# Kernel optimization log

Measured on AMD Instinct MI355X. Metric: run time of the kernel, lower is better.

## Reference

```python
import jax, jax.numpy as jnp
import numpy as np

N_NODES = 19385
N_EDGES = 1_200_000
GNN = 256
HID = 512
RANK = 512
NCLS = 3
NGENES = 6640
NBLK = 6
B = 256
EPS = 1e-5


def _ln(x, g, b):
    m = jnp.mean(x, axis=-1, keepdims=True)
    v = jnp.mean(jnp.square(x - m), axis=-1, keepdims=True)
    return (x - m) * jax.lax.rsqrt(v + EPS) * g + b


def setup_inputs() -> dict:
    key = jax.random.key(0)
    ks = iter(jax.random.split(key, 40))
    w = lambda shape, s=0.02: jax.random.normal(next(ks), shape, jnp.float32) * s
    inp = {
        'node_idx': jax.random.randint(next(ks), (B,), -1, N_NODES),  # -1 == OOV
        'edge_index': jax.random.randint(next(ks), (2, N_EDGES), 0, N_NODES),
        'edge_weight': jax.random.uniform(next(ks), (N_EDGES,), jnp.float32),
        'frozen_emb': jax.random.normal(next(ks), (N_NODES, GNN), jnp.float32),
        # trainable partial GNN (mps.6, mps.7, post_mp)
        'conv6_W': w((GNN, GNN)), 'conv6_b': jnp.zeros((GNN,)),
        'ln6_g': jnp.ones((GNN,)), 'ln6_b': jnp.zeros((GNN,)),
        'conv7_W': w((GNN, GNN)), 'conv7_b': jnp.zeros((GNN,)),
        'ln7_g': jnp.ones((GNN,)), 'ln7_b': jnp.zeros((GNN,)),
        'post_W': w((GNN, GNN)), 'post_b': jnp.zeros((GNN,)),
        # head
        'oov_emb': w((GNN,)),
        'in_ln_g': jnp.ones((GNN,)), 'in_ln_b': jnp.zeros((GNN,)),
        'proj_in_W': w((GNN, HID)), 'proj_in_b': jnp.zeros((HID,)),
        'rb_ln_g': jnp.ones((NBLK, HID)), 'rb_ln_b': jnp.zeros((NBLK, HID)),
        'rb_W1': w((NBLK, HID, 4 * HID)), 'rb_b1': jnp.zeros((NBLK, 4 * HID)),
        'rb_W2': w((NBLK, 4 * HID, HID)), 'rb_b2': jnp.zeros((NBLK, HID)),
        'out_ln_g': jnp.ones((HID,)), 'out_ln_b': jnp.zeros((HID,)),
        'bil_W': w((HID, NCLS * RANK)), 'bil_b': jnp.zeros((NCLS * RANK,)),
        'out_gene_emb': w((NGENES, RANK)),
    }
    return inp


def reference(node_idx, edge_index, edge_weight, frozen_emb,
              conv6_W, conv6_b, ln6_g, ln6_b,
              conv7_W, conv7_b, ln7_g, ln7_b,
              post_W, post_b,
              oov_emb, in_ln_g, in_ln_b, proj_in_W, proj_in_b,
              rb_ln_g, rb_ln_b, rb_W1, rb_b1, rb_W2, rb_b2,
              out_ln_g, out_ln_b, bil_W, bil_b, out_gene_emb):
    src, dst = edge_index[0], edge_index[1]

    def conv(x, W, b):
        # edge-weighted message passing: gather -> scale -> scatter-add -> linear
        msg = x[src] * edge_weight[:, None]              # [E, GNN]
        agg = jax.ops.segment_sum(msg, dst, num_segments=N_NODES)
        return agg @ W + b

    # trainable GNN layers (eval mode: dropout = identity)
    x = frozen_emb
    x = x + jax.nn.relu(_ln(conv(x, conv6_W, conv6_b), ln6_g, ln6_b))
    x = x + jax.nn.relu(_ln(conv(x, conv7_W, conv7_b), ln7_g, ln7_b))
    node_emb = x @ post_W + post_b                       # [N, GNN]

    # OOV-aware lookup
    in_f = (node_idx >= 0).astype(jnp.float32)[:, None]  # [B,1]
    gnn_emb = node_emb[jnp.clip(node_idx, 0, None)]      # [B, GNN]
    h = gnn_emb * in_f + oov_emb[None, :] * (1.0 - in_f)

    # MLP head
    h = _ln(h, in_ln_g, in_ln_b) @ proj_in_W + proj_in_b
    for i in range(NBLK):
        t = _ln(h, rb_ln_g[i], rb_ln_b[i])
        t = jax.nn.gelu(t @ rb_W1[i] + rb_b1[i])
        h = h + t @ rb_W2[i] + rb_b2[i]
    h = _ln(h, out_ln_g, out_ln_b)

    pert = (h @ bil_W + bil_b).reshape(B, NCLS, RANK)
    logits = jnp.einsum('bcr,gr->bcg', pert, out_gene_emb)  # [B, 3, 6640]
    return logits
```

## Files before the change

### kernel.cpp

```cpp
#include <hip/hip_runtime.h>
#include <hip/hip_bf16.h>
#include <cstdint>
#include <cstddef>

#define N_NODES_C 19385
#define N_EDGES_C 1200000
#define GNN_C 256
#define HID_C 512
#define RANK_C 512
#define NCLS_C 3
#define NGENES_C 6640
#define NBLK_C 6
#define B_C 256
#define LN_EPS 1e-5f

#define PH_K 256
#define PH_CHUNK ((N_EDGES_C + PH_K - 1) / PH_K)
#define PH_NW ((N_NODES_C + 1) / 2)

typedef short bf8v __attribute__((ext_vector_type(8)));
typedef float f4v __attribute__((ext_vector_type(4)));
typedef int i2v __attribute__((ext_vector_type(2)));

__device__ __forceinline__ float bfu2f(unsigned short u) {
  union { unsigned int i; float f; } c; c.i = ((unsigned)u) << 16; return c.f;
}
__device__ __forceinline__ unsigned short f2bfu(float v) {
  union { float f; unsigned u; } c; c.f = v;
  unsigned r = c.u + 0x7FFFu + ((c.u >> 16) & 1u);
  return (unsigned short)(r >> 16);
}
__device__ __forceinline__ float gelu_tanh(float v) {
  const float x3 = v * v * v;
  return 0.5f * v * (1.f + tanhf(0.7978845608028654f * (v + 0.044715f * x3)));
}


struct CvtSeg { const float* s; unsigned short* d; long long n; };
struct CvtArgs { CvtSeg seg[2]; int nseg; };

__global__ __launch_bounds__(256) void multicvt_kernel(CvtArgs a) {
  for (int sg = 0; sg < a.nseg; ++sg) {
    const float4* s = reinterpret_cast<const float4*>(a.seg[sg].s);
    unsigned short* d = a.seg[sg].d;
    const long long n4 = a.seg[sg].n >> 2;
    for (long long i = blockIdx.x * 256 + threadIdx.x; i < n4;
         i += (long long)gridDim.x * 256) {
      float4 v = s[i];
      ushort4 o;
      o.x = f2bfu(v.x); o.y = f2bfu(v.y); o.z = f2bfu(v.z); o.w = f2bfu(v.w);
      *reinterpret_cast<ushort4*>(d + i * 4) = o;
    }
  }
}


struct TSeg { const float* s; unsigned short* d; int R, C; };
struct TArgs { TSeg seg[12]; int nseg; };

__global__ __launch_bounds__(256) void multitrans_kernel(TArgs a) {
  __shared__ float tile[32][33];
  const int tx = threadIdx.x & 31;
  const int ty = threadIdx.x >> 5;
  for (int sg = 0; sg < a.nseg; ++sg) {
    const int R = a.seg[sg].R, C = a.seg[sg].C;
    const int tC = C >> 5;
    const int nt = (R >> 5) * tC;
    const float* src = a.seg[sg].s;
    unsigned short* dst = a.seg[sg].d;
    for (int tid = blockIdx.x; tid < nt; tid += gridDim.x) {
      const int tr = tid / tC, tc = tid - tr * tC;
      const int r0 = tr * 32, c0 = tc * 32;
      __syncthreads();
#pragma unroll
      for (int j = 0; j < 32; j += 8)
        tile[ty + j][tx] = src[(size_t)(r0 + ty + j) * C + c0 + tx];
      __syncthreads();
#pragma unroll
      for (int j = 0; j < 32; j += 8)
        dst[(size_t)(c0 + ty + j) * R + r0 + tx] = f2bfu(tile[tx][ty + j]);
    }
  }
}


__global__ __launch_bounds__(256) void initmark_kernel(const int* __restrict__ node_idx,
                                                       int* __restrict__ selbm,
                                                       int* __restrict__ needed) {
  __shared__ int sel[B_C];
  sel[threadIdx.x] = max(node_idx[threadIdx.x], 0);
  __syncthreads();
  for (int i = blockIdx.x * 256 + threadIdx.x; i < N_NODES_C;
       i += gridDim.x * 256) {
    int m = 0;
#pragma unroll 16
    for (int j = 0; j < B_C; ++j) m |= (sel[j] == i);
    selbm[i] = m;
    needed[i] = m;
  }
}

__global__ __launch_bounds__(1024) void privhist_kernel(const int* __restrict__ src,
                                                        const int* __restrict__ dst,
                                                        const int* __restrict__ selbm,
                                                        int* __restrict__ needed,
                                                        unsigned int* __restrict__ cntp) {
  __shared__ unsigned int bins[PH_NW];
  const int t = threadIdx.x;
  for (int w = t; w < PH_NW; w += 1024) bins[w] = 0u;
  __syncthreads();
  const int base = blockIdx.x * PH_CHUNK;
  const int end = min(base + PH_CHUNK, N_EDGES_C);
#pragma unroll 2
  for (int i = base + t; i < end; i += 1024) {
    const int d = dst[i];
    atomicAdd(&bins[d >> 1], 1u << ((d & 1) * 16));
    if (selbm[d]) needed[src[i]] = 1;
  }
  __syncthreads();
  unsigned int* out = cntp + (size_t)blockIdx.x * PH_NW;
  for (int w = t; w < PH_NW; w += 1024) out[w] = bins[w];
}

__global__ __launch_bounds__(256) void redhist_kernel(unsigned int* __restrict__ cntp,
                                                      int* __restrict__ cnt) {
  const int w = blockIdx.x * 256 + threadIdx.x;
  if (w >= PH_NW) return;
  unsigned int lo = 0, hi = 0;
#pragma unroll 4
  for (int k = 0; k < PH_K; ++k) {
    const size_t idx = (size_t)k * PH_NW + w;
    const unsigned int u = cntp[idx];
    cntp[idx] = lo | (hi << 16);
    lo += u & 0xFFFFu;
    hi += u >> 16;
  }
  cnt[2 * w] = (int)lo;
  if (2 * w + 1 < N_NODES_C) cnt[2 * w + 1] = (int)hi;
}

__global__ __launch_bounds__(1024) void scan_kernel(const int* __restrict__ cnt,
                                                    int* __restrict__ off, int n) {
  __shared__ int sums[1024];
  const int t = threadIdx.x;
  const int CH = (n + 1023) >> 10;
  const int base = t * CH;
  int s = 0;
  for (int i = 0; i < CH; ++i) {
    int idx = base + i;
    if (idx < n) s += cnt[idx];
  }
  sums[t] = s;
  __syncthreads();
  for (int d = 1; d < 1024; d <<= 1) {
    int v = (t >= d) ? sums[t - d] : 0;
    __syncthreads();
    sums[t] += v;
    __syncthreads();
  }
  int run = (t == 0) ? 0 : sums[t - 1];
  for (int i = 0; i < CH; ++i) {
    int idx = base + i;
    if (idx < n) { off[idx] = run; run += cnt[idx]; }
  }
  if (t == 0) off[n] = sums[1023];
}

__global__ __launch_bounds__(1024) void fill_kernel(const int* __restrict__ src,
                                                    const int* __restrict__ dst,
                                                    const float* __restrict__ ew,
                                                    const int* __restrict__ off,
                                                    const unsigned int* __restrict__ cntp,
                                                    const int* __restrict__ needed,
                                                    i2v* __restrict__ ep) {
  __shared__ unsigned int bins[PH_NW];
  const int t = threadIdx.x;
  const unsigned int* myp = cntp + (size_t)blockIdx.x * PH_NW;
  for (int w = t; w < PH_NW; w += 1024) bins[w] = myp[w];
  __syncthreads();
  const int base = blockIdx.x * PH_CHUNK;
  const int end = min(base + PH_CHUNK, N_EDGES_C);
#pragma unroll 2
  for (int i = base + t; i < end; i += 1024) {
    const int d = dst[i];
    if (!needed[d]) continue;
    const int sh = (d & 1) * 16;
    const unsigned int old = atomicAdd(&bins[d >> 1], 1u << sh);
    const int rank = (int)((old >> sh) & 0xFFFFu);
    i2v e;
    e[0] = src[i] * GNN_C;
    e[1] = __float_as_int(ew[i]);
    ep[off[d] + rank] = e;
  }
}


__global__ __launch_bounds__(256) void agg_full_kernel(const i2v* __restrict__ ep,
                                                       const int* __restrict__ off,
                                                       const int* __restrict__ needed,
                                                       const unsigned short* __restrict__ x,
                                                       unsigned short* __restrict__ aggbf) {
  const int n = blockIdx.x;
  if (!needed[n]) return;
  __shared__ f4v red[4][64];
  const int t = threadIdx.x;
  const int w = __builtin_amdgcn_readfirstlane(t >> 6);
  const int lane = t & 63;
  const int s0 = off[n];
  const int c = off[n + 1] - s0;
  const int q0 = s0 + ((c * w) >> 2);
  const int q1 = s0 + ((c * (w + 1)) >> 2);
  float a0 = 0.f, a1 = 0.f, a2 = 0.f, a3 = 0.f;
  const unsigned short* xl = x + 4 * lane;
#pragma unroll 4
  for (int p = q0; p < q1; ++p) {
    const i2v e = ep[p];
    const int s = e[0];
    const float wg = __int_as_float(e[1]);
    const ushort4 v = *reinterpret_cast<const ushort4*>(xl + s);
    a0 = fmaf(bfu2f(v.x), wg, a0);
    a1 = fmaf(bfu2f(v.y), wg, a1);
    a2 = fmaf(bfu2f(v.z), wg, a2);
    a3 = fmaf(bfu2f(v.w), wg, a3);
  }
  f4v av; av[0] = a0; av[1] = a1; av[2] = a2; av[3] = a3;
  red[w][lane] = av;
  __syncthreads();
  const float* rf = reinterpret_cast<const float*>(red);
  const float sum = rf[t] + rf[256 + t] + rf[512 + t] + rf[768 + t];
  aggbf[(size_t)n * GNN_C + t] = f2bfu(sum);
}

__global__ __launch_bounds__(256) void agg_sel_kernel(const int* __restrict__ node_idx,
                                                      const i2v* __restrict__ ep,
                                                      const int* __restrict__ off,
                                                      const float* __restrict__ x,
                                                      unsigned short* __restrict__ aggbf) {
  __shared__ f4v red[4][64];
  const int b = blockIdx.x;
  const int t = threadIdx.x;
  const int n = max(node_idx[b], 0);
  const int w = __builtin_amdgcn_readfirstlane(t >> 6);
  const int lane = t & 63;
  const int s0 = off[n];
  const int c = off[n + 1] - s0;
  const int q0 = s0 + ((c * w) >> 2);
  const int q1 = s0 + ((c * (w + 1)) >> 2);
  float a0 = 0.f, a1 = 0.f, a2 = 0.f, a3 = 0.f;
  const float* xl = x + 4 * lane;
#pragma unroll 2
  for (int p = q0; p < q1; ++p) {
    const i2v e = ep[p];
    const int s = e[0];
    const float wg = __int_as_float(e[1]);
    const f4v v = *reinterpret_cast<const f4v*>(xl + s);
    a0 = fmaf(v[0], wg, a0);
    a1 = fmaf(v[1], wg, a1);
    a2 = fmaf(v[2], wg, a2);
    a3 = fmaf(v[3], wg, a3);
  }
  f4v av; av[0] = a0; av[1] = a1; av[2] = a2; av[3] = a3;
  red[w][lane] = av;
  __syncthreads();
  const float* rf = reinterpret_cast<const float*>(red);
  const float sum = rf[t] + rf[256 + t] + rf[512 + t] + rf[768 + t];
  aggbf[(size_t)b * GNN_C + t] = f2bfu(sum);
}


#define MBK 32
#define MLDW 40

__global__ __launch_bounds__(256) void mgemm_kernel(const unsigned short* __restrict__ A,
                                                    const unsigned short* __restrict__ Bt,
                                                    const float* __restrict__ bias,
                                                    float* __restrict__ C,
                                                    int M, int N, int K) {
  __shared__ unsigned short As[128][MLDW];
  __shared__ unsigned short Bs[128][MLDW];
  const int t = threadIdx.x;
  const int lane = t & 63;
  const int wave = t >> 6;
  const int r0 = blockIdx.x * 128;
  const int c0 = blockIdx.y * 128;
  const int wm = (wave >> 1) * 64;
  const int wn = (wave & 1) * 64;
  const int lm = lane & 15;
  const int lq = lane >> 4;

  f4v acc[4][4];
  for (int i = 0; i < 4; ++i)
    for (int j = 0; j < 4; ++j)
      for (int r = 0; r < 4; ++r) acc[i][j][r] = 0.f;

  const int row = t >> 1;
  const int kof = (t & 1) * 16;
  for (int k0 = 0; k0 < K; k0 += MBK) {
    {
      const int gr = r0 + row;
      uint4 u0 = make_uint4(0, 0, 0, 0), u1 = u0;
      if (gr < M) {
        const uint4* p = reinterpret_cast<const uint4*>(A + (size_t)gr * K + k0 + kof);
        u0 = p[0]; u1 = p[1];
      }
      *reinterpret_cast<uint4*>(&As[row][kof]) = u0;
      *reinterpret_cast<uint4*>(&As[row][kof + 8]) = u1;
    }
    {
      const int gn = c0 + row;
      uint4 u0 = make_uint4(0, 0, 0, 0), u1 = u0;
      if (gn < N) {
        const uint4* p = reinterpret_cast<const uint4*>(Bt + (size_t)gn * K + k0 + kof);
        u0 = p[0]; u1 = p[1];
      }
      *reinterpret_cast<uint4*>(&Bs[row][kof]) = u0;
      *reinterpret_cast<uint4*>(&Bs[row][kof + 8]) = u1;
    }
    __syncthreads();

    bf8v a[4], b[4];
#pragma unroll
    for (int i = 0; i < 4; ++i)
      a[i] = *reinterpret_cast<const bf8v*>(&As[wm + i * 16 + lm][lq * 8]);
#pragma unroll
    for (int j = 0; j < 4; ++j)
      b[j] = *reinterpret_cast<const bf8v*>(&Bs[wn + j * 16 + lm][lq * 8]);
#pragma unroll
    for (int i = 0; i < 4; ++i)
#pragma unroll
      for (int j = 0; j < 4; ++j)
        acc[i][j] = __builtin_amdgcn_mfma_f32_16x16x32_bf16(a[i], b[j], acc[i][j], 0, 0, 0);
    __syncthreads();
  }

  for (int ti = 0; ti < 4; ++ti) {
    for (int tj = 0; tj < 4; ++tj) {
      const int col = c0 + wn + tj * 16 + lm;
      if (col >= N) continue;
      const float bv = bias ? bias[col] : 0.f;
      for (int r = 0; r < 4; ++r) {
        const int row2 = r0 + wm + ti * 16 + lq * 4 + r;
        if (row2 < M) C[(size_t)row2 * N + col] = acc[ti][tj][r] + bv;
      }
    }
  }
}


__global__ __launch_bounds__(256) void mgemm32_kernel(const unsigned short* __restrict__ A,
                                                      const unsigned short* __restrict__ Bt,
                                                      const float* __restrict__ bias,
                                                      float* outF, unsigned short* outB,
                                                      int M, int N, int K, int doGelu) {
  __shared__ unsigned short As[32][MLDW];
  __shared__ unsigned short Bs[64][MLDW];
  const int t = threadIdx.x;
  const int lane = t & 63;
  const int wave = t >> 6;
  const int r0 = blockIdx.x * 32;
  const int c0 = blockIdx.y * 64;
  const int wn = wave * 16;
  const int lm = lane & 15;
  const int lq = lane >> 4;

  f4v acc[2];
#pragma unroll
  for (int i = 0; i < 2; ++i)
#pragma unroll
    for (int r = 0; r < 4; ++r) acc[i][r] = 0.f;

  const int arow = t >> 3, akof = (t & 7) * 4;
  const int brow = t >> 2, bkof = (t & 3) * 8;
  for (int k0 = 0; k0 < K; k0 += MBK) {
    *reinterpret_cast<ushort4*>(&As[arow][akof]) =
        *reinterpret_cast<const ushort4*>(A + (size_t)(r0 + arow) * K + k0 + akof);
    *reinterpret_cast<uint4*>(&Bs[brow][bkof]) =
        *reinterpret_cast<const uint4*>(Bt + (size_t)(c0 + brow) * K + k0 + bkof);
    __syncthreads();
    bf8v a[2], b;
#pragma unroll
    for (int i = 0; i < 2; ++i)
      a[i] = *reinterpret_cast<const bf8v*>(&As[i * 16 + lm][lq * 8]);
    b = *reinterpret_cast<const bf8v*>(&Bs[wn + lm][lq * 8]);
#pragma unroll
    for (int i = 0; i < 2; ++i)
      acc[i] = __builtin_amdgcn_mfma_f32_16x16x32_bf16(a[i], b, acc[i], 0, 0, 0);
    __syncthreads();
  }

  const int col = c0 + wn + lm;
  const float bv = bias ? bias[col] : 0.f;
#pragma unroll
  for (int ti = 0; ti < 2; ++ti)
#pragma unroll
    for (int r = 0; r < 4; ++r) {
      const int row2 = r0 + ti * 16 + lq * 4 + r;
      float v = acc[ti][r] + bv;
      if (doGelu) v = gelu_tanh(v);
      if (outF) outF[(size_t)row2 * N + col] = v;
      else outB[(size_t)row2 * N + col] = f2bfu(v);
    }
}

__global__ __launch_bounds__(256) void skmgemm32_kernel(const unsigned short* __restrict__ A,
                                                        const unsigned short* __restrict__ Bt,
                                                        float* __restrict__ part,
                                                        int M, int N, int K, int kc) {
  __shared__ unsigned short As[32][MLDW];
  __shared__ unsigned short Bs[64][MLDW];
  const int t = threadIdx.x;
  const int lane = t & 63;
  const int wave = t >> 6;
  const int r0 = blockIdx.x * 32;
  const int c0 = blockIdx.y * 64;
  const int kBeg = blockIdx.z * kc;
  const int kEnd = kBeg + kc;
  const int wn = wave * 16;
  const int lm = lane & 15;
  const int lq = lane >> 4;

  f4v acc[2];
#pragma unroll
  for (int i = 0; i < 2; ++i)
#pragma unroll
    for (int r = 0; r < 4; ++r) acc[i][r] = 0.f;

  const int arow = t >> 3, akof = (t & 7) * 4;
  const int brow = t >> 2, bkof = (t & 3) * 8;
  for (int k0 = kBeg; k0 < kEnd; k0 += MBK) {
    *reinterpret_cast<ushort4*>(&As[arow][akof]) =
        *reinterpret_cast<const ushort4*>(A + (size_t)(r0 + arow) * K + k0 + akof);
    *reinterpret_cast<uint4*>(&Bs[brow][bkof]) =
        *reinterpret_cast<const uint4*>(Bt + (size_t)(c0 + brow) * K + k0 + bkof);
    __syncthreads();
    bf8v a[2], b;
#pragma unroll
    for (int i = 0; i < 2; ++i)
      a[i] = *reinterpret_cast<const bf8v*>(&As[i * 16 + lm][lq * 8]);
    b = *reinterpret_cast<const bf8v*>(&Bs[wn + lm][lq * 8]);
#pragma unroll
    for (int i = 0; i < 2; ++i)
      acc[i] = __builtin_amdgcn_mfma_f32_16x16x32_bf16(a[i], b, acc[i], 0, 0, 0);
    __syncthreads();
  }

  float* out = part + (size_t)blockIdx.z * M * N;
  const int col = c0 + wn + lm;
#pragma unroll
  for (int ti = 0; ti < 2; ++ti)
#pragma unroll
    for (int r = 0; r < 4; ++r) {
      const int row2 = r0 + ti * 16 + lq * 4 + r;
      out[(size_t)row2 * N + col] = acc[ti][r];
    }
}

__global__ __launch_bounds__(512) void gemmln6_kernel(const unsigned short* __restrict__ A,
                                                      const unsigned short* __restrict__ Bt,
                                                      const float* __restrict__ bias,
                                                      const float* __restrict__ g,
                                                      const float* __restrict__ b,
                                                      const float* __restrict__ frozen,
                                                      const int* __restrict__ needed,
                                                      float* __restrict__ yx, int M) {
  __shared__ unsigned short As[32][MLDW];
  __shared__ unsigned short Bs[256][MLDW];
  __shared__ float rs[32][8];
  const int t = threadIdx.x;
  const int lane = t & 63;
  const int wave = t >> 6;
  const int r0 = blockIdx.x * 32;
  const int lm = lane & 15, lq = lane >> 4;

  f4v acc[2][2];
#pragma unroll
  for (int i = 0; i < 2; ++i)
#pragma unroll
    for (int j = 0; j < 2; ++j)
#pragma unroll
      for (int r = 0; r < 4; ++r) acc[i][j][r] = 0.f;

  const int arow = t >> 3, akof = (t & 7) * 4;
  for (int k0 = 0; k0 < GNN_C; k0 += MBK) {
    if (t < 256) {
      ushort4 u = make_ushort4(0, 0, 0, 0);
      const int gr = r0 + arow;
      if (gr < M) u = *reinterpret_cast<const ushort4*>(A + (size_t)gr * GNN_C + k0 + akof);
      *reinterpret_cast<ushort4*>(&As[arow][akof]) = u;
    }
#pragma unroll
    for (int j = 0; j < 2; ++j) {
      const int id = t + 512 * j;
      const int brow = id >> 2, bkof = (id & 3) * 8;
      *reinterpret_cast<uint4*>(&Bs[brow][bkof]) =
          *reinterpret_cast<const uint4*>(Bt + (size_t)brow * GNN_C + k0 + bkof);
    }
    __syncthreads();
    bf8v a[2], bf[2];
#pragma unroll
    for (int ti = 0; ti < 2; ++ti)
      a[ti] = *reinterpret_cast<const bf8v*>(&As[ti * 16 + lm][lq * 8]);
#pragma unroll
    for (int tj = 0; tj < 2; ++tj)
      bf[tj] = *reinterpret_cast<const bf8v*>(&Bs[wave * 32 + tj * 16 + lm][lq * 8]);
#pragma unroll
    for (int ti = 0; ti < 2; ++ti)
#pragma unroll
      for (int tj = 0; tj < 2; ++tj)
        acc[ti][tj] = __builtin_amdgcn_mfma_f32_16x16x32_bf16(a[ti], bf[tj], acc[ti][tj], 0, 0, 0);
    __syncthreads();
  }

  const int c0 = wave * 32 + lm, c1 = c0 + 16;
  const float b0 = bias[c0], b1 = bias[c1];
#pragma unroll
  for (int ti = 0; ti < 2; ++ti)
#pragma unroll
    for (int r = 0; r < 4; ++r) { acc[ti][0][r] += b0; acc[ti][1][r] += b1; }

  float m[2][4];
#pragma unroll
  for (int ti = 0; ti < 2; ++ti)
#pragma unroll
    for (int r = 0; r < 4; ++r) {
      float s = acc[ti][0][r] + acc[ti][1][r];
      for (int o = 1; o < 16; o <<= 1) s += __shfl_xor(s, o, 64);
      if (lm == 0) rs[ti * 16 + lq * 4 + r][wave] = s;
    }
  __syncthreads();
#pragma unroll
  for (int ti = 0; ti < 2; ++ti)
#pragma unroll
    for (int r = 0; r < 4; ++r) {
      const int row = ti * 16 + lq * 4 + r;
      float s = 0.f;
#pragma unroll
      for (int w2 = 0; w2 < 8; ++w2) s += rs[row][w2];
      m[ti][r] = s * (1.f / GNN_C);
    }
  __syncthreads();
  float iv[2][4];
#pragma unroll
  for (int ti = 0; ti < 2; ++ti)
#pragma unroll
    for (int r = 0; r < 4; ++r) {
      const float d0 = acc[ti][0][r] - m[ti][r];
      const float d1 = acc[ti][1][r] - m[ti][r];
      float s = d0 * d0 + d1 * d1;
      for (int o = 1; o < 16; o <<= 1) s += __shfl_xor(s, o, 64);
      if (lm == 0) rs[ti * 16 + lq * 4 + r][wave] = s;
    }
  __syncthreads();
#pragma unroll
  for (int ti = 0; ti < 2; ++ti)
#pragma unroll
    for (int r = 0; r < 4; ++r) {
      const int row = ti * 16 + lq * 4 + r;
      float s = 0.f;
#pragma unroll
      for (int w2 = 0; w2 < 8; ++w2) s += rs[row][w2];
      iv[ti][r] = rsqrtf(s * (1.f / GNN_C) + LN_EPS);
    }

  const float g0 = g[c0], g1 = g[c1], bb0 = b[c0], bb1 = b[c1];
#pragma unroll
  for (int ti = 0; ti < 2; ++ti)
#pragma unroll
    for (int r = 0; r < 4; ++r) {
      const int grow = r0 + ti * 16 + lq * 4 + r;
      if (grow < M && needed[grow]) {
        const size_t base = (size_t)grow * GNN_C;
        const float x0 = fmaxf((acc[ti][0][r] - m[ti][r]) * iv[ti][r] * g0 + bb0, 0.f);
        const float x1 = fmaxf((acc[ti][1][r] - m[ti][r]) * iv[ti][r] * g1 + bb1, 0.f);
        yx[base + c0] = frozen[base + c0] + x0;
        yx[base + c1] = frozen[base + c1] + x1;
      }
    }
}


__global__ __launch_bounds__(256) void postconv7_kernel(const float* __restrict__ y,
                                                        const float* __restrict__ g,
                                                        const float* __restrict__ b,
                                                        const int* __restrict__ idx,
                                                        const float* __restrict__ x1f,
                                                        unsigned short* __restrict__ out) {
  __shared__ float sb[4];
  const int bi = blockIdx.x, t = threadIdx.x;
  const int n = max(idx[bi], 0);
  const float v = y[(size_t)bi * GNN_C + t];
  float s = v;
  for (int o = 32; o; o >>= 1) s += __shfl_down(s, o, 64);
  if ((t & 63) == 0) sb[t >> 6] = s;
  __syncthreads();
  const float m = (sb[0] + sb[1] + sb[2] + sb[3]) * (1.f / GNN_C);
  __syncthreads();
  const float d = v - m;
  s = d * d;
  for (int o = 32; o; o >>= 1) s += __shfl_down(s, o, 64);
  if ((t & 63) == 0) sb[t >> 6] = s;
  __syncthreads();
  const float rs = rsqrtf((sb[0] + sb[1] + sb[2] + sb[3]) * (1.f / GNN_C) + LN_EPS);
  const float xn = d * rs * g[t] + b[t];
  out[(size_t)bi * GNN_C + t] = f2bfu(x1f[(size_t)n * GNN_C + t] + fmaxf(xn, 0.f));
}

__global__ __launch_bounds__(256) void h0ln_kernel(const float* __restrict__ ne,
                                                   const int* __restrict__ idx,
                                                   const float* __restrict__ oov,
                                                   const float* __restrict__ g,
                                                   const float* __restrict__ b,
                                                   unsigned short* __restrict__ out) {
  __shared__ float sb[4];
  const int bi = blockIdx.x, t = threadIdx.x;
  const float v = (idx[bi] >= 0) ? ne[(size_t)bi * GNN_C + t] : oov[t];
  float s = v;
  for (int o = 32; o; o >>= 1) s += __shfl_down(s, o, 64);
  if ((t & 63) == 0) sb[t >> 6] = s;
  __syncthreads();
  const float m = (sb[0] + sb[1] + sb[2] + sb[3]) * (1.f / GNN_C);
  __syncthreads();
  const float d = v - m;
  s = d * d;
  for (int o = 32; o; o >>= 1) s += __shfl_down(s, o, 64);
  if ((t & 63) == 0) sb[t >> 6] = s;
  __syncthreads();
  const float rs = rsqrtf((sb[0] + sb[1] + sb[2] + sb[3]) * (1.f / GNN_C) + LN_EPS);
  out[(size_t)bi * GNN_C + t] = f2bfu(d * rs * g[t] + b[t]);
}

__global__ __launch_bounds__(256) void lnbf_kernel(const float* __restrict__ in,
                                                   const float* __restrict__ g,
                                                   const float* __restrict__ b,
                                                   unsigned short* __restrict__ out) {
  __shared__ float sb[4];
  const int r = blockIdx.x, t = threadIdx.x;
  const float v0 = in[(size_t)r * HID_C + t];
  const float v1 = in[(size_t)r * HID_C + t + 256];
  float s = v0 + v1;
  for (int o = 32; o; o >>= 1) s += __shfl_down(s, o, 64);
  if ((t & 63) == 0) sb[t >> 6] = s;
  __syncthreads();
  const float m = (sb[0] + sb[1] + sb[2] + sb[3]) * (1.f / HID_C);
  __syncthreads();
  const float d0 = v0 - m, d1 = v1 - m;
  s = d0 * d0 + d1 * d1;
  for (int o = 32; o; o >>= 1) s += __shfl_down(s, o, 64);
  if ((t & 63) == 0) sb[t >> 6] = s;
  __syncthreads();
  const float rs = rsqrtf((sb[0] + sb[1] + sb[2] + sb[3]) * (1.f / HID_C) + LN_EPS);
  out[(size_t)r * HID_C + t] = f2bfu(d0 * rs * g[t] + b[t]);
  out[(size_t)r * HID_C + t + 256] = f2bfu(d1 * rs * g[t + 256] + b[t + 256]);
}

__global__ __launch_bounds__(256) void combln_kernel(const float* __restrict__ part,
                                                     float* __restrict__ h,
                                                     const float* __restrict__ b2,
                                                     const float* __restrict__ g,
                                                     const float* __restrict__ b,
                                                     unsigned short* __restrict__ out) {
  __shared__ float sb[4];
  const int r = blockIdx.x, t = threadIdx.x;
  const int MN = B_C * HID_C;
  const size_t o0 = (size_t)r * HID_C + t;
  const size_t o1 = o0 + 256;
  float v0 = h[o0] + b2[t] + part[o0] + part[MN + o0] + part[2 * MN + o0] + part[3 * MN + o0];
  float v1 = h[o1] + b2[t + 256] + part[o1] + part[MN + o1] + part[2 * MN + o1] + part[3 * MN + o1];
  h[o0] = v0;
  h[o1] = v1;
  float s = v0 + v1;
  for (int o = 32; o; o >>= 1) s += __shfl_down(s, o, 64);
  if ((t & 63) == 0) sb[t >> 6] = s;
  __syncthreads();
  const float m = (sb[0] + sb[1] + sb[2] + sb[3]) * (1.f / HID_C);
  __syncthreads();
  const float d0 = v0 - m, d1 = v1 - m;
  s = d0 * d0 + d1 * d1;
  for (int o = 32; o; o >>= 1) s += __shfl_down(s, o, 64);
  if ((t & 63) == 0) sb[t >> 6] = s;
  __syncthreads();
  const float rsq = rsqrtf((sb[0] + sb[1] + sb[2] + sb[3]) * (1.f / HID_C) + LN_EPS);
  out[o0] = f2bfu(d0 * rsq * g[t] + b[t]);
  out[o1] = f2bfu(d1 * rsq * g[t + 256] + b[t + 256]);
}


extern "C" void kernel_launch(void* const* d_in, const int* in_sizes, int n_in,
                              void* d_out, int out_size, void* d_ws, size_t ws_size,
                              hipStream_t stream) {
  const int* node_idx = (const int*)d_in[0];
  const int* e_src = (const int*)d_in[1];
  const int* e_dst = e_src + N_EDGES_C;
  const float* ew = (const float*)d_in[2];
  const float* frozen = (const float*)d_in[3];
  const float* W6 = (const float*)d_in[4];
  const float* b6 = (const float*)d_in[5];
  const float* g6 = (const float*)d_in[6];
  const float* bl6 = (const float*)d_in[7];
  const float* W7 = (const float*)d_in[8];
  const float* b7 = (const float*)d_in[9];
  const float* g7 = (const float*)d_in[10];
  const float* bl7 = (const float*)d_in[11];
  const float* postW = (const float*)d_in[12];
  const float* postb = (const float*)d_in[13];
  const float* oov = (const float*)d_in[14];
  const float* ing = (const float*)d_in[15];
  const float* inb = (const float*)d_in[16];
  const float* projW = (const float*)d_in[17];
  const float* projb = (const float*)d_in[18];
  const float* rbg = (const float*)d_in[19];
  const float* rbb = (const float*)d_in[20];
  const float* rbW1 = (const float*)d_in[21];
  const float* rbb1 = (const float*)d_in[22];
  const float* rbW2 = (const float*)d_in[23];
  const float* rbb2 = (const float*)d_in[24];
  const float* outg = (const float*)d_in[25];
  const float* outb = (const float*)d_in[26];
  const float* bilW = (const float*)d_in[27];
  const float* bilb = (const float*)d_in[28];
  const float* gene = (const float*)d_in[29];
  (void)in_sizes; (void)n_in; (void)out_size; (void)ws_size;

  char* ws = (char*)d_ws;
  size_t o = 0;
  auto alloc = [&](size_t bytes) -> char* {
    char* p = ws + o;
    o += (bytes + 255) & ~(size_t)255;
    return p;
  };
  int* cnt = (int*)alloc((size_t)N_NODES_C * 4);
  int* off = (int*)alloc((size_t)(N_NODES_C + 1) * 4);
  int* needed = (int*)alloc((size_t)N_NODES_C * 4);
  int* selbm = (int*)alloc((size_t)N_NODES_C * 4);
  unsigned int* cntp = (unsigned int*)alloc((size_t)PH_K * PH_NW * 4);
  i2v* ep = (i2v*)alloc((size_t)N_EDGES_C * 8);
  unsigned short* frozbf = (unsigned short*)alloc((size_t)N_NODES_C * GNN_C * 2);
  char* aggregion = alloc((size_t)NBLK_C * HID_C * 4 * HID_C * 2);
  unsigned short* w6t = (unsigned short*)alloc((size_t)GNN_C * GNN_C * 2);
  unsigned short* w7t = (unsigned short*)alloc((size_t)GNN_C * GNN_C * 2);
  unsigned short* postWt = (unsigned short*)alloc((size_t)GNN_C * GNN_C * 2);
  unsigned short* projWt = (unsigned short*)alloc((size_t)HID_C * GNN_C * 2);
  unsigned short* bilWt = (unsigned short*)alloc((size_t)NCLS_C * RANK_C * HID_C * 2);
  float* yx = (float*)alloc((size_t)N_NODES_C * GNN_C * 4);
  unsigned short* rbW2t = (unsigned short*)alloc((size_t)NBLK_C * 4 * HID_C * HID_C * 2);
  float* part = (float*)alloc((size_t)4 * B_C * HID_C * 4);
  unsigned short* agg7bf = (unsigned short*)alloc((size_t)B_C * GNN_C * 2);
  float* y7b = (float*)alloc((size_t)B_C * GNN_C * 4);
  unsigned short* x2bf = (unsigned short*)alloc((size_t)B_C * GNN_C * 2);
  float* nemb = (float*)alloc((size_t)B_C * GNN_C * 4);
  unsigned short* h0lbf = (unsigned short*)alloc((size_t)B_C * GNN_C * 2);
  float* h = (float*)alloc((size_t)B_C * HID_C * 4);
  unsigned short* tbf = (unsigned short*)alloc((size_t)B_C * HID_C * 2);
  unsigned short* ubf = (unsigned short*)alloc((size_t)B_C * 4 * HID_C * 2);
  unsigned short* pertbf = (unsigned short*)alloc((size_t)B_C * NCLS_C * RANK_C * 2);

  unsigned short* agg6bf = (unsigned short*)aggregion;
  unsigned short* rbW1t = (unsigned short*)aggregion;
  unsigned short* genebf = frozbf;

  initmark_kernel<<<80, 256, 0, stream>>>(node_idx, selbm, needed);
  privhist_kernel<<<PH_K, 1024, 0, stream>>>(e_src, e_dst, selbm, needed, cntp);
  redhist_kernel<<<(PH_NW + 255) / 256, 256, 0, stream>>>(cntp, cnt);
  scan_kernel<<<1, 1024, 0, stream>>>(cnt, off, N_NODES_C);
  fill_kernel<<<PH_K, 1024, 0, stream>>>(e_src, e_dst, ew, off, cntp, needed, ep);

  {
    CvtArgs a;
    a.seg[0] = {frozen, frozbf, (long long)N_NODES_C * GNN_C};
    a.nseg = 1;
    multicvt_kernel<<<512, 256, 0, stream>>>(a);
  }
  {
    TArgs a;
    a.seg[0] = {W6, w6t, GNN_C, GNN_C};
    a.seg[1] = {W7, w7t, GNN_C, GNN_C};
    a.seg[2] = {postW, postWt, GNN_C, GNN_C};
    a.seg[3] = {projW, projWt, GNN_C, HID_C};
    a.seg[4] = {bilW, bilWt, HID_C, NCLS_C * RANK_C};
    a.nseg = 5;
    multitrans_kernel<<<512, 256, 0, stream>>>(a);
  }

  agg_full_kernel<<<N_NODES_C, 256, 0, stream>>>(ep, off, needed, frozbf, agg6bf);
  gemmln6_kernel<<<(N_NODES_C + 31) / 32, 512, 0, stream>>>(agg6bf, w6t, b6, g6, bl6,
                                                            frozen, needed, yx, N_NODES_C);

  {
    TArgs a;
    for (int i = 0; i < NBLK_C; ++i) {
      a.seg[i] = {rbW1 + (size_t)i * HID_C * 4 * HID_C,
                  rbW1t + (size_t)i * HID_C * 4 * HID_C, HID_C, 4 * HID_C};
      a.seg[6 + i] = {rbW2 + (size_t)i * 4 * HID_C * HID_C,
                      rbW2t + (size_t)i * 4 * HID_C * HID_C, 4 * HID_C, HID_C};
    }
    a.nseg = 12;
    multitrans_kernel<<<2048, 256, 0, stream>>>(a);
  }
  {
    CvtArgs a;
    a.seg[0] = {gene, genebf, (long long)NGENES_C * RANK_C};
    a.nseg = 1;
    multicvt_kernel<<<512, 256, 0, stream>>>(a);
  }

  agg_sel_kernel<<<B_C, 256, 0, stream>>>(node_idx, ep, off, yx, agg7bf);
  {
    dim3 g(B_C / 32, GNN_C / 64);
    mgemm32_kernel<<<g, 256, 0, stream>>>(agg7bf, w7t, b7, y7b, nullptr,
                                          B_C, GNN_C, GNN_C, 0);
  }
  postconv7_kernel<<<B_C, 256, 0, stream>>>(y7b, g7, bl7, node_idx, yx, x2bf);

  {
    dim3 g(B_C / 32, GNN_C / 64);
    mgemm32_kernel<<<g, 256, 0, stream>>>(x2bf, postWt, postb, nemb, nullptr,
                                          B_C, GNN_C, GNN_C, 0);
  }
  h0ln_kernel<<<B_C, 256, 0, stream>>>(nemb, node_idx, oov, ing, inb, h0lbf);

  {
    dim3 g(B_C / 32, HID_C / 64);
    mgemm32_kernel<<<g, 256, 0, stream>>>(h0lbf, projWt, projb, h, nullptr,
                                          B_C, HID_C, GNN_C, 0);
  }
  lnbf_kernel<<<B_C, 256, 0, stream>>>(h, rbg, rbb, tbf);

  for (int i = 0; i < NBLK_C; ++i) {
    {
      dim3 g(B_C / 32, (4 * HID_C) / 64);
      mgemm32_kernel<<<g, 256, 0, stream>>>(tbf, rbW1t + (size_t)i * HID_C * 4 * HID_C,
                                            rbb1 + (size_t)i * 4 * HID_C, nullptr, ubf,
                                            B_C, 4 * HID_C, HID_C, 1);
    }
    {
      dim3 g(B_C / 32, HID_C / 64, 4);
      skmgemm32_kernel<<<g, 256, 0, stream>>>(ubf, rbW2t + (size_t)i * 4 * HID_C * HID_C,
                                              part, B_C, HID_C, 4 * HID_C, HID_C);
    }
    const float* gn = (i < NBLK_C - 1) ? rbg + (size_t)(i + 1) * HID_C : outg;
    const float* bn = (i < NBLK_C - 1) ? rbb + (size_t)(i + 1) * HID_C : outb;
    combln_kernel<<<B_C, 256, 0, stream>>>(part, h, rbb2 + (size_t)i * HID_C, gn, bn, tbf);
  }

  {
    dim3 g(B_C / 32, (NCLS_C * RANK_C) / 64);
    mgemm32_kernel<<<g, 256, 0, stream>>>(tbf, bilWt, bilb, nullptr, pertbf,
                                          B_C, NCLS_C * RANK_C, HID_C, 0);
  }

  {
    dim3 g((B_C * NCLS_C) / 128, (NGENES_C + 127) / 128);
    mgemm_kernel<<<g, 256, 0, stream>>>(pertbf, genebf, nullptr, (float*)d_out,
                                        B_C * NCLS_C, NGENES_C, RANK_C);
  }
}
```

Baseline: 551.6 us.

## Fuse residual MLP stack into one cooperative kernel with grid syncs

Replaces the 18 per-block kernel launches (W1 GEMM+GELU, split-K W2 GEMM, combine+LayerNorm) with a single cooperative kernel of 256 blocks that loops over the six residual blocks and separates the stages with grid-wide barriers. The aim is to remove launch overhead and inter-kernel gaps for these small GEMMs. In exchange it adds grid.sync cost, and the launch depends on all 256 blocks being co-resident. The launch return value is ignored.

```diff
diff --git a/kernel.cpp b/kernel.cpp
--- a/kernel.cpp
+++ b/kernel.cpp
@@ -1,7 +1,10 @@
 #include <hip/hip_runtime.h>
 #include <hip/hip_bf16.h>
+#include <hip/hip_cooperative_groups.h>
 #include <cstdint>
 #include <cstddef>
+
+namespace cg = cooperative_groups;
 
 #define N_NODES_C 19385
 #define N_EDGES_C 1200000
@@ -402,57 +405,125 @@
     }
 }
 
-__global__ __launch_bounds__(256) void skmgemm32_kernel(const unsigned short* __restrict__ A,
-                                                        const unsigned short* __restrict__ Bt,
-                                                        float* __restrict__ part,
-                                                        int M, int N, int K, int kc) {
+__global__ __launch_bounds__(256) void resstack_kernel(
+    unsigned short* __restrict__ tbf, unsigned short* __restrict__ ubf,
+    float* __restrict__ part, float* __restrict__ h,
+    const unsigned short* __restrict__ rbW1t, const float* __restrict__ rbb1,
+    const unsigned short* __restrict__ rbW2t, const float* __restrict__ rbb2,
+    const float* __restrict__ rbg, const float* __restrict__ rbb,
+    const float* __restrict__ outg, const float* __restrict__ outb) {
   __shared__ unsigned short As[32][MLDW];
   __shared__ unsigned short Bs[64][MLDW];
+  __shared__ float sb[4];
+  cg::grid_group grid = cg::this_grid();
   const int t = threadIdx.x;
   const int lane = t & 63;
   const int wave = t >> 6;
-  const int r0 = blockIdx.x * 32;
-  const int c0 = blockIdx.y * 64;
-  const int kBeg = blockIdx.z * kc;
-  const int kEnd = kBeg + kc;
+  const int lm = lane & 15, lq = lane >> 4;
   const int wn = wave * 16;
-  const int lm = lane & 15;
-  const int lq = lane >> 4;
-
-  f4v acc[2];
-#pragma unroll
-  for (int i = 0; i < 2; ++i)
-#pragma unroll
-    for (int r = 0; r < 4; ++r) acc[i][r] = 0.f;
-
+  const int blk = blockIdx.x;
   const int arow = t >> 3, akof = (t & 7) * 4;
   const int brow = t >> 2, bkof = (t & 3) * 8;
-  for (int k0 = kBeg; k0 < kEnd; k0 += MBK) {
-    *reinterpret_cast<ushort4*>(&As[arow][akof]) =
-        *reinterpret_cast<const ushort4*>(A + (size_t)(r0 + arow) * K + k0 + akof);
-    *reinterpret_cast<uint4*>(&Bs[brow][bkof]) =
-        *reinterpret_cast<const uint4*>(Bt + (size_t)(c0 + brow) * K + k0 + bkof);
-    __syncthreads();
-    bf8v a[2], b;
-#pragma unroll
-    for (int i = 0; i < 2; ++i)
-      a[i] = *reinterpret_cast<const bf8v*>(&As[i * 16 + lm][lq * 8]);
-    b = *reinterpret_cast<const bf8v*>(&Bs[wn + lm][lq * 8]);
-#pragma unroll
-    for (int i = 0; i < 2; ++i)
-      acc[i] = __builtin_amdgcn_mfma_f32_16x16x32_bf16(a[i], b, acc[i], 0, 0, 0);
-    __syncthreads();
-  }
-
-  float* out = part + (size_t)blockIdx.z * M * N;
-  const int col = c0 + wn + lm;
-#pragma unroll
-  for (int ti = 0; ti < 2; ++ti)
-#pragma unroll
-    for (int r = 0; r < 4; ++r) {
-      const int row2 = r0 + ti * 16 + lq * 4 + r;
-      out[(size_t)row2 * N + col] = acc[ti][r];
-    }
+
+  for (int i = 0; i < NBLK_C; ++i) {
+    {
+      const unsigned short* W1 = rbW1t + (size_t)i * HID_C * 4 * HID_C;
+      const float* b1 = rbb1 + (size_t)i * 4 * HID_C;
+      const int r0 = (blk >> 5) * 32;
+      const int c0 = (blk & 31) * 64;
+      f4v acc[2];
+#pragma unroll
+      for (int q = 0; q < 2; ++q)
+#pragma unroll
+        for (int r = 0; r < 4; ++r) acc[q][r] = 0.f;
+      for (int k0 = 0; k0 < HID_C; k0 += MBK) {
+        *reinterpret_cast<ushort4*>(&As[arow][akof]) =
+            *reinterpret_cast<const ushort4*>(tbf + (size_t)(r0 + arow) * HID_C + k0 + akof);
+        *reinterpret_cast<uint4*>(&Bs[brow][bkof]) =
+            *reinterpret_cast<const uint4*>(W1 + (size_t)(c0 + brow) * HID_C + k0 + bkof);
+        __syncthreads();
+        bf8v a0 = *reinterpret_cast<const bf8v*>(&As[lm][lq * 8]);
+        bf8v a1 = *reinterpret_cast<const bf8v*>(&As[16 + lm][lq * 8]);
+        bf8v b = *reinterpret_cast<const bf8v*>(&Bs[wn + lm][lq * 8]);
+        acc[0] = __builtin_amdgcn_mfma_f32_16x16x32_bf16(a0, b, acc[0], 0, 0, 0);
+        acc[1] = __builtin_amdgcn_mfma_f32_16x16x32_bf16(a1, b, acc[1], 0, 0, 0);
+        __syncthreads();
+      }
+      const int col = c0 + wn + lm;
+      const float bv = b1[col];
+#pragma unroll
+      for (int q = 0; q < 2; ++q)
+#pragma unroll
+        for (int r = 0; r < 4; ++r) {
+          const int row2 = r0 + q * 16 + lq * 4 + r;
+          ubf[(size_t)row2 * (4 * HID_C) + col] = f2bfu(gelu_tanh(acc[q][r] + bv));
+        }
+    }
+    grid.sync();
+    {
+      const unsigned short* W2 = rbW2t + (size_t)i * 4 * HID_C * HID_C;
+      const int z = blk >> 6;
+      const int rc = blk & 63;
+      const int r0 = (rc >> 3) * 32;
+      const int c0 = (rc & 7) * 64;
+      const int kBeg = z * HID_C;
+      f4v acc[2];
+#pragma unroll
+      for (int q = 0; q < 2; ++q)
+#pragma unroll
+        for (int r = 0; r < 4; ++r) acc[q][r] = 0.f;
+      for (int k0 = kBeg; k0 < kBeg + HID_C; k0 += MBK) {
+        *reinterpret_cast<ushort4*>(&As[arow][akof]) =
+            *reinterpret_cast<const ushort4*>(ubf + (size_t)(r0 + arow) * (4 * HID_C) + k0 + akof);
+        *reinterpret_cast<uint4*>(&Bs[brow][bkof]) =
+            *reinterpret_cast<const uint4*>(W2 + (size_t)(c0 + brow) * (4 * HID_C) + k0 + bkof);
+        __syncthreads();
+        bf8v a0 = *reinterpret_cast<const bf8v*>(&As[lm][lq * 8]);
+        bf8v a1 = *reinterpret_cast<const bf8v*>(&As[16 + lm][lq * 8]);
+        bf8v b = *reinterpret_cast<const bf8v*>(&Bs[wn + lm][lq * 8]);
+        acc[0] = __builtin_amdgcn_mfma_f32_16x16x32_bf16(a0, b, acc[0], 0, 0, 0);
+        acc[1] = __builtin_amdgcn_mfma_f32_16x16x32_bf16(a1, b, acc[1], 0, 0, 0);
+        __syncthreads();
+      }
+      float* out = part + (size_t)z * B_C * HID_C;
+      const int col = c0 + wn + lm;
+#pragma unroll
+      for (int q = 0; q < 2; ++q)
+#pragma unroll
+        for (int r = 0; r < 4; ++r) {
+          const int row2 = r0 + q * 16 + lq * 4 + r;
+          out[(size_t)row2 * HID_C + col] = acc[q][r];
+        }
+    }
+    grid.sync();
+    {
+      const float* b2 = rbb2 + (size_t)i * HID_C;
+      const float* gn = (i < NBLK_C - 1) ? rbg + (size_t)(i + 1) * HID_C : outg;
+      const float* bn = (i < NBLK_C - 1) ? rbb + (size_t)(i + 1) * HID_C : outb;
+      const int MN = B_C * HID_C;
+      const size_t o0 = (size_t)blk * HID_C + t;
+      const size_t o1 = o0 + 256;
+      float v0 = h[o0] + b2[t] + part[o0] + part[MN + o0] + part[2 * MN + o0] + part[3 * MN + o0];
+      float v1 = h[o1] + b2[t + 256] + part[o1] + part[MN + o1] + part[2 * MN + o1] + part[3 * MN + o1];
+      h[o0] = v0;
+      h[o1] = v1;
+      float s = v0 + v1;
+      for (int o = 32; o; o >>= 1) s += __shfl_down(s, o, 64);
+      if ((t & 63) == 0) sb[t >> 6] = s;
+      __syncthreads();
+      const float m = (sb[0] + sb[1] + sb[2] + sb[3]) * (1.f / HID_C);
+      __syncthreads();
+      const float d0 = v0 - m, d1 = v1 - m;
+      s = d0 * d0 + d1 * d1;
+      for (int o = 32; o; o >>= 1) s += __shfl_down(s, o, 64);
+      if ((t & 63) == 0) sb[t >> 6] = s;
+      __syncthreads();
+      const float rsq = rsqrtf((sb[0] + sb[1] + sb[2] + sb[3]) * (1.f / HID_C) + LN_EPS);
+      tbf[o0] = f2bfu(d0 * rsq * gn[t] + bn[t]);
+      tbf[o1] = f2bfu(d1 * rsq * gn[t + 256] + bn[t + 256]);
+    }
+    grid.sync();
+  }
 }
 
 __global__ __launch_bounds__(512) void gemmln6_kernel(const unsigned short* __restrict__ A,
@@ -651,37 +722,6 @@
   const float rs = rsqrtf((sb[0] + sb[1] + sb[2] + sb[3]) * (1.f / HID_C) + LN_EPS);
   out[(size_t)r * HID_C + t] = f2bfu(d0 * rs * g[t] + b[t]);
   out[(size_t)r * HID_C + t + 256] = f2bfu(d1 * rs * g[t + 256] + b[t + 256]);
-}
-
-__global__ __launch_bounds__(256) void combln_kernel(const float* __restrict__ part,
-                                                     float* __restrict__ h,
-                                                     const float* __restrict__ b2,
-                                                     const float* __restrict__ g,
-                                                     const float* __restrict__ b,
-                                                     unsigned short* __restrict__ out) {
-  __shared__ float sb[4];
-  const int r = blockIdx.x, t = threadIdx.x;
-  const int MN = B_C * HID_C;
-  const size_t o0 = (size_t)r * HID_C + t;
-  const size_t o1 = o0 + 256;
-  float v0 = h[o0] + b2[t] + part[o0] + part[MN + o0] + part[2 * MN + o0] + part[3 * MN + o0];
-  float v1 = h[o1] + b2[t + 256] + part[o1] + part[MN + o1] + part[2 * MN + o1] + part[3 * MN + o1];
-  h[o0] = v0;
-  h[o1] = v1;
-  float s = v0 + v1;
-  for (int o = 32; o; o >>= 1) s += __shfl_down(s, o, 64);
-  if ((t & 63) == 0) sb[t >> 6] = s;
-  __syncthreads();
-  const float m = (sb[0] + sb[1] + sb[2] + sb[3]) * (1.f / HID_C);
-  __syncthreads();
-  const float d0 = v0 - m, d1 = v1 - m;
-  s = d0 * d0 + d1 * d1;
-  for (int o = 32; o; o >>= 1) s += __shfl_down(s, o, 64);
-  if ((t & 63) == 0) sb[t >> 6] = s;
-  __syncthreads();
-  const float rsq = rsqrtf((sb[0] + sb[1] + sb[2] + sb[3]) * (1.f / HID_C) + LN_EPS);
-  out[o0] = f2bfu(d0 * rsq * g[t] + b[t]);
-  out[o1] = f2bfu(d1 * rsq * g[t + 256] + b[t + 256]);
 }
 
 
@@ -825,21 +865,11 @@
   }
   lnbf_kernel<<<B_C, 256, 0, stream>>>(h, rbg, rbb, tbf);
 
-  for (int i = 0; i < NBLK_C; ++i) {
-    {
-      dim3 g(B_C / 32, (4 * HID_C) / 64);
-      mgemm32_kernel<<<g, 256, 0, stream>>>(tbf, rbW1t + (size_t)i * HID_C * 4 * HID_C,
-                                            rbb1 + (size_t)i * 4 * HID_C, nullptr, ubf,
-                                            B_C, 4 * HID_C, HID_C, 1);
-    }
-    {
-      dim3 g(B_C / 32, HID_C / 64, 4);
-      skmgemm32_kernel<<<g, 256, 0, stream>>>(ubf, rbW2t + (size_t)i * 4 * HID_C * HID_C,
-                                              part, B_C, HID_C, 4 * HID_C, HID_C);
-    }
-    const float* gn = (i < NBLK_C - 1) ? rbg + (size_t)(i + 1) * HID_C : outg;
-    const float* bn = (i < NBLK_C - 1) ? rbb + (size_t)(i + 1) * HID_C : outb;
-    combln_kernel<<<B_C, 256, 0, stream>>>(part, h, rbb2 + (size_t)i * HID_C, gn, bn, tbf);
+  {
+    void* args[] = {&tbf, &ubf, &part, &h, &rbW1t, &rbb1, &rbW2t, &rbb2,
+                    &rbg, &rbb, &outg, &outb};
+    (void)hipLaunchCooperativeKernel(reinterpret_cast<void*>(resstack_kernel),
+                                     dim3(256), dim3(256), args, 0, stream);
   }
 
   {
```

Result: slower. 1.096 ms (+98.6%).
